# Kernel tuning notes

Hardware: AMD Instinct MI355X
Metric: run time of the kernel (lower is better)

The kernel has to match this reference:

```python
import jax, jax.numpy as jnp
import numpy as np

B, D_in, D_hid, D_out, D_future = 1024, 1024, 1024, 512, 32


def _lin_init(key, out_d, in_d, k_scale):
    k = 1.0 / np.sqrt(k_scale)
    k1, k2 = jax.random.split(key)
    W = jax.random.uniform(k1, (out_d, in_d), minval=-k, maxval=k, dtype=jnp.float32)
    b = jax.random.uniform(k2, (out_d,), minval=-k, maxval=k, dtype=jnp.float32)
    return W, b


def _lstm_cell(x, h, c, W_ih, W_hh, b_ih, b_hh):
    # PyTorch LSTMCell gate order: i, f, g, o
    gates = x @ W_ih.T + b_ih + h @ W_hh.T + b_hh
    i, f, g, o = jnp.split(gates, 4, axis=1)
    c2 = jax.nn.sigmoid(f) * c + jax.nn.sigmoid(i) * jnp.tanh(g)
    h2 = jax.nn.sigmoid(o) * jnp.tanh(c2)
    return h2, c2


def setup_inputs() -> dict:
    key = jax.random.key(0)
    ks = jax.random.split(key, 16)
    x = jax.random.normal(ks[0], (B, D_in), dtype=jnp.float32)
    hx = jax.random.normal(ks[1], (B, D_hid), dtype=jnp.float32)
    cx = jax.random.normal(ks[2], (B, D_hid), dtype=jnp.float32)
    # Decoder LSTMCell(D_out -> D_hid); torch init scale 1/sqrt(hidden)
    W_ih_dec, b_ih_dec = _lin_init(ks[3], 4 * D_hid, D_out, D_hid)
    W_hh_dec, b_hh_dec = _lin_init(ks[4], 4 * D_hid, D_hid, D_hid)
    W_r0, b_r0 = _lin_init(ks[5], D_hid, D_hid, D_hid)
    W_rp, b_rp = _lin_init(ks[6], D_out, D_hid, D_hid)
    W_rr, b_rr = _lin_init(ks[7], D_out, D_out, D_out)
    W_s0, b_s0 = _lin_init(ks[8], D_in, D_hid, D_hid)
    # StaRNNCell LSTMCell(2*D_in -> D_hid)
    W_ih_sta, b_ih_sta = _lin_init(ks[9], 4 * D_hid, 2 * D_in, D_hid)
    W_hh_sta, b_hh_sta = _lin_init(ks[10], 4 * D_hid, D_hid, D_hid)
    W_sn, b_sn = _lin_init(ks[11], D_out, D_hid, D_hid)
    return dict(x=x, hx=hx, cx=cx,
                W_ih_dec=W_ih_dec, W_hh_dec=W_hh_dec, b_ih_dec=b_ih_dec, b_hh_dec=b_hh_dec,
                W_r0=W_r0, b_r0=b_r0, W_rp=W_rp, b_rp=b_rp, W_rr=W_rr, b_rr=b_rr,
                W_s0=W_s0, b_s0=b_s0,
                W_ih_sta=W_ih_sta, W_hh_sta=W_hh_sta, b_ih_sta=b_ih_sta, b_hh_sta=b_hh_sta,
                W_sn=W_sn, b_sn=b_sn)


def reference(x, hx, cx,
              W_ih_dec, W_hh_dec, b_ih_dec, b_hh_dec,
              W_r0, b_r0, W_rp, b_rp, W_rr, b_rr,
              W_s0, b_s0,
              W_ih_sta, W_hh_sta, b_ih_sta, b_hh_sta,
              W_sn, b_sn):
    ohx, ocx = hx, cx
    r0 = jnp.zeros((x.shape[0], D_out), dtype=x.dtype)
    hd0 = hx @ W_r0.T + b_r0  # LinLayerR0

    def step(carry, _):
        r, hd, cd = carry
        hd, cd = _lstm_cell(r, hd, cd, W_ih_dec, W_hh_dec, b_ih_dec, b_hh_dec)
        p = hd @ W_rp.T + b_rp    # LinLayerRp
        r = p @ W_rr.T + b_rr     # LinLayerRr
        return (r, hd, cd), (hd, p)

    _, (fts_bar, Act_bar) = jax.lax.scan(step, (r0, hd0, cx), None, length=D_future)
    # fts_bar: [D_future, B, D_hid]; AvgPool1d over D_future == mean over axis 0
    hbar = fts_bar.mean(axis=0)
    xbar = jax.nn.relu(hbar @ W_s0.T + b_s0)  # LinLayerS0 + relu
    xcat = jnp.concatenate([x, xbar], axis=1)
    hx2, cx2 = _lstm_cell(xcat, ohx, ocx, W_ih_sta, W_hh_sta, b_ih_sta, b_hh_sta)
    Act = hx2 @ W_sn.T + b_sn  # LinLayerSn
    return (Act, Act_bar, (hx2, cx2))
```

## Files before the change

kernel.cpp:

```cpp
#include <hip/hip_runtime.h>
#include <hip/hip_bf16.h>
#include <stdint.h>


typedef unsigned short ushort_t;
typedef __attribute__((ext_vector_type(8))) short short8;
typedef __attribute__((ext_vector_type(4))) float floatx4;

__device__ __forceinline__ unsigned short f2bf(float f) {
    unsigned int u = __float_as_uint(f);
    u += 0x7FFF + ((u >> 16) & 1);
    return (unsigned short)(u >> 16);
}
__device__ __forceinline__ float bf2f(unsigned short u) {
    return __uint_as_float(((unsigned int)u) << 16);
}
__device__ __forceinline__ float sigm(float x) { return 1.f / (1.f + __expf(-x)); }

__device__ __forceinline__ void glds16(const ushort_t* g, const ushort_t* l) {
    __builtin_amdgcn_global_load_lds(
        (const __attribute__((address_space(1))) uint32_t*)g,
        (__attribute__((address_space(3))) uint32_t*)l, 16, 0, 0);
}

template <bool WF, bool WB, bool RELU, bool NT>
__global__ __launch_bounds__(256)
void gemm_bt(const ushort_t* __restrict__ A, int lda,
             const ushort_t* __restrict__ Bw, int ldb,
             int Kloop, int kzOff,
             const float* __restrict__ bias,
             float* __restrict__ Cf, int ldcf, size_t czStride,
             ushort_t* __restrict__ Cb, int ldcb) {
    __shared__ __align__(16) ushort_t As[128 * 32];
    __shared__ __align__(16) ushort_t Bs[128 * 32];
    const int t = threadIdx.x;
    const int l = t & 63;
    const int w = t >> 6;
    int bx = blockIdx.x, by = blockIdx.y;
    if ((gridDim.y & 7) == 0) {
        const int flat = bx + gridDim.x * by;
        const int xcd = flat & 7;
        const int j = flat >> 3;
        const int jm = j / gridDim.x;
        by = xcd * (gridDim.y >> 3) + jm;
        bx = j - jm * gridDim.x;
    }
    const int m0 = by << 7;
    const int n0 = bx << 7;
    const int kz = blockIdx.z;
    A  += (size_t)kz * kzOff;
    Bw += (size_t)kz * kzOff;
    if (WF) Cf += (size_t)kz * czStride;
    const int wm = (w >> 1) << 6;
    const int wn = (w & 1) << 6;
    const int lr = l & 15;
    const int lg = l >> 4;

    floatx4 acc[4][4] = {};

    const int srow = (w << 4) + (l >> 2);
    const int cc = ((l & 3) - ((l >> 3) & 3)) & 3;
    const int scol = cc << 3;
    const ushort_t* Ag0 = A + (size_t)(m0 + srow) * lda + scol;
    const ushort_t* Ag1 = A + (size_t)(m0 + 64 + srow) * lda + scol;
    const ushort_t* Bg0 = Bw + (size_t)(n0 + srow) * ldb + scol;
    const ushort_t* Bg1 = Bw + (size_t)(n0 + 64 + srow) * ldb + scol;
    const ushort_t* lA0 = &As[t * 8];
    const ushort_t* lA1 = &As[2048 + t * 8];
    const ushort_t* lB0 = &Bs[t * 8];
    const ushort_t* lB1 = &Bs[2048 + t * 8];

    int aoff[4], boff[4];
#pragma unroll
    for (int i = 0; i < 4; i++) {
        const int Ra = wm + i * 16 + lr;
        aoff[i] = ((Ra << 2) + ((lg + ((Ra >> 1) & 3)) & 3)) << 3;
        const int Rb = wn + i * 16 + lr;
        boff[i] = ((Rb << 2) + ((lg + ((Rb >> 1) & 3)) & 3)) << 3;
    }

    for (int kk = 0; kk < Kloop; kk += 32) {
        glds16(Ag0 + kk, lA0);
        glds16(Ag1 + kk, lA1);
        glds16(Bg0 + kk, lB0);
        glds16(Bg1 + kk, lB1);
        __syncthreads();
        short8 af[4], bfr[4];
#pragma unroll
        for (int i = 0; i < 4; i++) af[i] = *(const short8*)&As[aoff[i]];
#pragma unroll
        for (int j = 0; j < 4; j++) bfr[j] = *(const short8*)&Bs[boff[j]];
#pragma unroll
        for (int i = 0; i < 4; i++)
#pragma unroll
            for (int j = 0; j < 4; j++)
                acc[i][j] = __builtin_amdgcn_mfma_f32_16x16x32_bf16(af[i], bfr[j], acc[i][j], 0, 0, 0);
        __syncthreads();
    }

#pragma unroll
    for (int i = 0; i < 4; i++) {
#pragma unroll
        for (int j = 0; j < 4; j++) {
            const int col = n0 + wn + j * 16 + lr;
            const float bv = bias ? bias[col] : 0.f;
#pragma unroll
            for (int r = 0; r < 4; r++) {
                const int row = m0 + wm + i * 16 + lg * 4 + r;
                float v = acc[i][j][r] + bv;
                if (RELU) v = fmaxf(v, 0.f);
                if (WF) {
                    if (NT) __builtin_nontemporal_store(v, &Cf[(size_t)row * ldcf + col]);
                    else Cf[(size_t)row * ldcf + col] = v;
                }
                if (WB) Cb[(size_t)row * ldcb + col] = f2bf(v);
            }
        }
    }
}

template <bool HF, bool NT>
__global__ __launch_bounds__(256, 2)
void gates_fused(const ushort_t* __restrict__ A, int lda,
                 const ushort_t* __restrict__ WI, int K,
                 const float* __restrict__ biasI,
                 const float* __restrict__ cin, float* __restrict__ cout,
                 ushort_t* __restrict__ hbf, int ldh,
                 float* __restrict__ hf) {
    __shared__ __align__(16) float Cs[64 * 132];
    ushort_t* AsBase = (ushort_t*)Cs;
    const int t = threadIdx.x;
    const int l = t & 63;
    const int w = t >> 6;
    const int flat = blockIdx.x + (blockIdx.y << 5);
    const int xcd = flat & 7;
    const int jsw = flat >> 3;
    const int bn = (xcd << 2) + (jsw >> 4);
    const int bm = jsw & 15;
    const int m0 = bm << 6;
    const int n0 = bn << 7;
    const int u0 = bn << 5;
    const int lr = l & 15;
    const int lg = l >> 4;

    floatx4 acc[4][2] = {};

    const int srow = t >> 2;
    const int cc = ((t & 3) - ((t >> 3) & 3)) & 3;
    const int scol = cc << 3;
    const ushort_t* Ag = A + (size_t)(m0 + srow) * lda + scol;

    int aoff[4];
#pragma unroll
    for (int i = 0; i < 4; i++) {
        const int Ra = i * 16 + lr;
        aoff[i] = ((Ra << 2) + ((lg + ((Ra >> 1) & 3)) & 3)) << 3;
    }
    const ushort_t* BgW[2];
#pragma unroll
    for (int jf = 0; jf < 2; jf++)
        BgW[jf] = WI + (size_t)(n0 + (w << 5) + jf * 16 + lr) * K + (lg << 3);

    auto issueA = [&](int b, int sp) {
#pragma unroll
        for (int s = 0; s < 4; s++)
            glds16(Ag + sp * 128 + s * 32, AsBase + b * 8192 + s * 2048 + t * 8);
    };
    auto loadB = [&](short8 (&br)[4][2], int sp) {
#pragma unroll
        for (int s = 0; s < 4; s++)
#pragma unroll
            for (int jf = 0; jf < 2; jf++)
                br[s][jf] = *(const short8*)(BgW[jf] + sp * 128 + s * 32);
    };
    auto compute = [&](int b, short8 (&br)[4][2]) {
#pragma unroll
        for (int s = 0; s < 4; s++) {
            short8 af[4];
#pragma unroll
            for (int i = 0; i < 4; i++)
                af[i] = *(const short8*)(AsBase + b * 8192 + s * 2048 + aoff[i]);
#pragma unroll
            for (int i = 0; i < 4; i++)
#pragma unroll
                for (int jf = 0; jf < 2; jf++)
                    acc[i][jf] = __builtin_amdgcn_mfma_f32_16x16x32_bf16(af[i], br[s][jf], acc[i][jf], 0, 0, 0);
        }
    };

    short8 b0[4][2], b1[4][2];
    const int NS = K >> 7;
    issueA(0, 0);
    loadB(b0, 0);
    for (int sp = 0; sp < NS; sp += 2) {
        __syncthreads();
        if (sp + 1 < NS) { issueA(1, sp + 1); loadB(b1, sp + 1); }
        compute(0, b0);
        __syncthreads();
        if (sp + 2 < NS) { issueA(0, sp + 2); loadB(b0, sp + 2); }
        compute(1, b1);
    }
    __syncthreads();

#pragma unroll
    for (int i = 0; i < 4; i++)
#pragma unroll
        for (int jf = 0; jf < 2; jf++) {
            const int colb = (w << 5) + jf * 16 + lr;
#pragma unroll
            for (int r = 0; r < 4; r++)
                Cs[(i * 16 + lg * 4 + r) * 132 + colb] = acc[i][jf][r];
        }
    __syncthreads();

#pragma unroll
    for (int p = 0; p < 8; p++) {
        const int row = p * 8 + (t >> 5);
        const int uu = t & 31;
        const float4 g4 = *(const float4*)&Cs[row * 132 + uu * 4];
        const int grow = m0 + row;
        const int gu = u0 + uu;
        const float4 b4 = *(const float4*)&biasI[gu * 4];
        const float iv = sigm(g4.x + b4.x);
        const float fv = sigm(g4.y + b4.y);
        const float gv = tanhf(g4.z + b4.z);
        const float ov = sigm(g4.w + b4.w);
        const size_t cidx = (size_t)grow * 1024 + gu;
        const float c = fv * cin[cidx] + iv * gv;
        const float h = ov * tanhf(c);
        if (NT) __builtin_nontemporal_store(c, &cout[cidx]);
        else cout[cidx] = c;
        hbf[(size_t)grow * ldh + gu] = f2bf(h);
        if (HF) {
            if (NT) __builtin_nontemporal_store(h, &hf[cidx]);
            else hf[cidx] = h;
        }
    }
}

__global__ void pack2_bf(ushort_t* __restrict__ dst, const float* __restrict__ s1, int K1,
                         const float* __restrict__ s2, int K2) {
    const int n = blockIdx.y;
    const int k = blockIdx.x * 256 + threadIdx.x;
    const int Kt = K1 + K2;
    float v = (k < K1) ? s1[(size_t)n * K1 + k] : s2[(size_t)n * K2 + (k - K1)];
    dst[(size_t)n * Kt + k] = f2bf(v);
}

__global__ void tpose_bf(ushort_t* __restrict__ dst, const float* __restrict__ src,
                         int R, int C) {
    const int c = blockIdx.y;
    const int r = blockIdx.x * 256 + threadIdx.x;
    dst[(size_t)c * R + r] = f2bf(src[(size_t)r * C + c]);
}

__global__ void ileave_whh_k(ushort_t* __restrict__ dst, const float* __restrict__ Whh) {
    const int rI = blockIdx.y;
    const int k = blockIdx.x * 256 + threadIdx.x;
    const int r = ((rI & 3) << 10) + (rI >> 2);
    dst[(size_t)rI * 1024 + k] = f2bf(Whh[(size_t)r * 1024 + k]);
}

__global__ void ileave_add_k(ushort_t* __restrict__ dst, const float* __restrict__ Wgf,
                             const float* __restrict__ Whh) {
    const int rI = blockIdx.y;
    const int k = blockIdx.x * 256 + threadIdx.x;
    const int r = ((rI & 3) << 10) + (rI >> 2);
    dst[(size_t)rI * 1024 + k] = f2bf(Wgf[(size_t)r * 1024 + k] + Whh[(size_t)r * 1024 + k]);
}

__global__ void ileave_sta_k(ushort_t* __restrict__ dst, const float* __restrict__ Wih,
                             const float* __restrict__ Whh) {
    const int rI = blockIdx.y;
    const int k = blockIdx.x * 256 + threadIdx.x;
    const int r = ((rI & 3) << 10) + (rI >> 2);
    float v = (k < 2048) ? Wih[(size_t)r * 2048 + k] : Whh[(size_t)r * 1024 + (k - 2048)];
    dst[(size_t)rI * 3072 + k] = f2bf(v);
}

__global__ void bias_il_k(float* __restrict__ dst, const float* __restrict__ b_ih,
                          const float* __restrict__ b_hh) {
    const int rI = blockIdx.x * 256 + threadIdx.x;
    const int r = ((rI & 3) << 10) + (rI >> 2);
    dst[rI] = b_ih[r] + b_hh[r];
}

__global__ void br2_k(float* __restrict__ br2, const float* __restrict__ Wrr,
                      const float* __restrict__ b_rp, const float* __restrict__ b_rr) {
    const int o = blockIdx.x * 256 + threadIdx.x;
    float s = b_rr[o];
    for (int m = 0; m < 512; m++) s += Wrr[o * 512 + m] * b_rp[m];
    br2[o] = s;
}

__global__ void biasg_k(float* __restrict__ dst, const float* __restrict__ Wih,
                        const float* __restrict__ b_ih, const float* __restrict__ b_hh,
                        const float* __restrict__ br2) {
    const int rI = blockIdx.x * 256 + threadIdx.x;
    const int r = ((rI & 3) << 10) + (rI >> 2);
    float s = b_ih[r] + b_hh[r];
    for (int o = 0; o < 512; o++) s += Wih[(size_t)r * 512 + o] * br2[o];
    dst[rI] = s;
}

__global__ void init_dec(const float* __restrict__ cx, float* __restrict__ cd) {
    int idx = blockIdx.x * 256 + threadIdx.x;
    cd[idx] = cx[idx];
}

__global__ void init_sta(const float* __restrict__ x, const float* __restrict__ hx,
                         ushort_t* __restrict__ A2) {
    int idx = blockIdx.x * 256 + threadIdx.x;
    int b = idx >> 10, j = idx & 1023;
    A2[(size_t)b * 3072 + j] = f2bf(x[idx]);
    A2[(size_t)b * 3072 + 2048 + j] = f2bf(hx[idx]);
}

__global__ void hbar_from_slots(const ushort_t* __restrict__ HD1,
                                ushort_t* __restrict__ out) {
    const size_t SLOT = 1048576;
    int idx = blockIdx.x * 256 + threadIdx.x;
    float s = 0.f;
#pragma unroll 8
    for (int t = 0; t < 32; t++) s += bf2f(HD1[(size_t)t * SLOT + idx]);
    out[idx] = f2bf(s * (1.f / 32.f));
}

extern "C" void kernel_launch(void* const* d_in, const int* in_sizes, int n_in,
                              void* d_out, int out_size, void* d_ws, size_t ws_size,
                              hipStream_t stream) {
    const float* x        = (const float*)d_in[0];
    const float* hx       = (const float*)d_in[1];
    const float* cx       = (const float*)d_in[2];
    const float* W_ih_dec = (const float*)d_in[3];
    const float* W_hh_dec = (const float*)d_in[4];
    const float* b_ih_dec = (const float*)d_in[5];
    const float* b_hh_dec = (const float*)d_in[6];
    const float* W_r0     = (const float*)d_in[7];
    const float* b_r0     = (const float*)d_in[8];
    const float* W_rp     = (const float*)d_in[9];
    const float* b_rp     = (const float*)d_in[10];
    const float* W_rr     = (const float*)d_in[11];
    const float* b_rr     = (const float*)d_in[12];
    const float* W_s0     = (const float*)d_in[13];
    const float* b_s0     = (const float*)d_in[14];
    const float* W_ih_sta = (const float*)d_in[15];
    const float* W_hh_sta = (const float*)d_in[16];
    const float* b_ih_sta = (const float*)d_in[17];
    const float* b_hh_sta = (const float*)d_in[18];
    const float* W_sn     = (const float*)d_in[19];
    const float* b_sn     = (const float*)d_in[20];
    float* out = (float*)d_out;

    float* Act    = out;
    float* ActBar = out + 524288;
    float* Hx2    = out + 524288 + 16777216;
    float* Cx2    = Hx2 + 1048576;

    char* ws = (char*)d_ws;
    size_t off = 0;
    auto alloc = [&](size_t bytes) -> void* {
        void* p = ws + off;
        off += (bytes + 255) & ~(size_t)255;
        return p;
    };
    const size_t SLOT = 1048576;
    ushort_t* HDall  = (ushort_t*)alloc(33ull * SLOT * 2);
    ushort_t* WgI    = (ushort_t*)alloc(4096ull * 1024 * 2);
    ushort_t* WcatSI = (ushort_t*)alloc(4096ull * 3072 * 2);
    ushort_t* Wrpb   = (ushort_t*)alloc(512ull * 1024 * 2);
    ushort_t* Wr0b   = (ushort_t*)alloc(1024ull * 1024 * 2);
    ushort_t* Ws0b   = (ushort_t*)alloc(1024ull * 1024 * 2);
    ushort_t* Wsnb   = (ushort_t*)alloc(512ull * 1024 * 2);
    float*    biasDI = (float*)alloc(4096 * 4);
    float*    biasGI = (float*)alloc(4096 * 4);
    float*    biasSI = (float*)alloc(4096 * 4);
    float*    br2    = (float*)alloc(512 * 4);
    ushort_t* Acat2  = (ushort_t*)alloc(1024ull * 3072 * 2);
    float*    cd     = (float*)alloc(1024ull * 1024 * 4);
    ushort_t* hbarb  = (ushort_t*)alloc(1024ull * 1024 * 2);
    ushort_t* hx2b   = (ushort_t*)alloc(1024ull * 1024 * 2);
    if (ws_size < off) return;

    float*    Wgf    = (float*)(HDall + 1 * SLOT);
    ushort_t* Wihb   = HDall + 9 * SLOT;
    ushort_t* WrpT   = HDall + 11 * SLOT;
    ushort_t* Wrp2Tb = HDall + 11 * SLOT + 524288;
    ushort_t* Wrrb   = HDall + 12 * SLOT;
    ushort_t* WhhI   = HDall + 13 * SLOT;

    init_dec<<<4096, 256, 0, stream>>>(cx, cd);
    init_sta<<<4096, 256, 0, stream>>>(x, hx, Acat2);
    pack2_bf<<<dim3(2, 512), 256, 0, stream>>>(Wrrb, W_rr, 512, nullptr, 0);
    pack2_bf<<<dim3(2, 4096), 256, 0, stream>>>(Wihb, W_ih_dec, 512, nullptr, 0);
    pack2_bf<<<dim3(4, 512), 256, 0, stream>>>(Wrpb, W_rp, 1024, nullptr, 0);
    pack2_bf<<<dim3(4, 1024), 256, 0, stream>>>(Wr0b, W_r0, 1024, nullptr, 0);
    pack2_bf<<<dim3(4, 1024), 256, 0, stream>>>(Ws0b, W_s0, 1024, nullptr, 0);
    pack2_bf<<<dim3(4, 512), 256, 0, stream>>>(Wsnb, W_sn, 1024, nullptr, 0);
    tpose_bf<<<dim3(2, 1024), 256, 0, stream>>>(WrpT, W_rp, 512, 1024);
    ileave_whh_k<<<dim3(4, 4096), 256, 0, stream>>>(WhhI, W_hh_dec);
    bias_il_k<<<16, 256, 0, stream>>>(biasDI, b_ih_dec, b_hh_dec);
    ileave_sta_k<<<dim3(12, 4096), 256, 0, stream>>>(WcatSI, W_ih_sta, W_hh_sta);
    bias_il_k<<<16, 256, 0, stream>>>(biasSI, b_ih_sta, b_hh_sta);
    br2_k<<<2, 256, 0, stream>>>(br2, W_rr, b_rp, b_rr);
    biasg_k<<<16, 256, 0, stream>>>(biasGI, W_ih_dec, b_ih_dec, b_hh_dec, br2);

    gemm_bt<false, true, false, false><<<dim3(4, 8, 1), 256, 0, stream>>>(
        WrpT, 512, Wrrb, 512, 512, 0, nullptr, nullptr, 0, 0, Wrp2Tb, 512);
    gemm_bt<true, false, false, false><<<dim3(8, 32, 1), 256, 0, stream>>>(
        Wihb, 512, Wrp2Tb, 512, 512, 0, nullptr, Wgf, 1024, 0, nullptr, 0);
    ileave_add_k<<<dim3(4, 4096), 256, 0, stream>>>(WgI, Wgf, W_hh_dec);

    gemm_bt<false, true, false, false><<<dim3(8, 8, 1), 256, 0, stream>>>(
        Acat2 + 2048, 3072, Wr0b, 1024, 1024, 0, b_r0, nullptr, 0, 0, HDall, 1024);

    for (int s = 0; s < 32; s++) {
        const ushort_t* WI = (s == 0) ? WhhI : WgI;
        const float* bI = (s == 0) ? biasDI : biasGI;
        gates_fused<false, false><<<dim3(32, 16), 256, 0, stream>>>(
            HDall + (size_t)s * SLOT, 1024, WI, 1024, bI,
            cd, cd, HDall + (size_t)(s + 1) * SLOT, 1024, nullptr);
    }

    gemm_bt<true, false, false, true><<<dim3(4, 256, 1), 256, 0, stream>>>(
        HDall + SLOT, 1024, Wrpb, 1024, 1024, 0, b_rp, ActBar, 512, 0, nullptr, 0);

    hbar_from_slots<<<4096, 256, 0, stream>>>(HDall + SLOT, hbarb);
    gemm_bt<false, true, true, false><<<dim3(8, 8, 1), 256, 0, stream>>>(
        hbarb, 1024, Ws0b, 1024, 1024, 0, b_s0, nullptr, 0, 0, Acat2 + 1024, 3072);

    gates_fused<true, true><<<dim3(32, 16), 256, 0, stream>>>(
        Acat2, 3072, WcatSI, 3072, biasSI, cx, Cx2, hx2b, 1024, Hx2);

    gemm_bt<true, false, false, true><<<dim3(4, 8, 1), 256, 0, stream>>>(
        hx2b, 1024, Wsnb, 1024, 1024, 0, b_sn, Act, 512, 0, nullptr, 0);

    (void)in_sizes; (void)n_in; (void)out_size;
}
```

Baseline: 1.238 ms.

## Replace per-step LSTM gate launches with a persistent kernel using grid barriers

The 32 sequential gate-kernel launches become one persistent kernel of 512 blocks that synchronises between timesteps with a global atomic barrier. The cell state stays in registers across steps, and the hidden-state mean is summed in registers, so the cell-state buffer round-trips, the init copy kernel and the separate hbar reduction kernel go away. This removes launch gaps and memory traffic, but it needs all 512 blocks to be co-resident (launch bounds 256,2) or the barrier deadlocks. Barrier latency is paid on every step.

```diff
diff --git a/kernel.cpp b/kernel.cpp
--- a/kernel.cpp
+++ b/kernel.cpp
@@ -21,6 +21,24 @@
     __builtin_amdgcn_global_load_lds(
         (const __attribute__((address_space(1))) uint32_t*)g,
         (__attribute__((address_space(3))) uint32_t*)l, 16, 0, 0);
+}
+
+__device__ __forceinline__ void grid_sync(unsigned* cnt, unsigned* gen) {
+    __syncthreads();
+    if (threadIdx.x == 0) {
+        __threadfence();
+        unsigned g = __hip_atomic_load(gen, __ATOMIC_RELAXED, __HIP_MEMORY_SCOPE_AGENT);
+        unsigned a = __hip_atomic_fetch_add(cnt, 1u, __ATOMIC_ACQ_REL, __HIP_MEMORY_SCOPE_AGENT);
+        if (a == 511u) {
+            __hip_atomic_store(cnt, 0u, __ATOMIC_RELAXED, __HIP_MEMORY_SCOPE_AGENT);
+            __hip_atomic_store(gen, g + 1u, __ATOMIC_RELEASE, __HIP_MEMORY_SCOPE_AGENT);
+        } else {
+            while (__hip_atomic_load(gen, __ATOMIC_ACQUIRE, __HIP_MEMORY_SCOPE_AGENT) == g)
+                __builtin_amdgcn_s_sleep(8);
+        }
+        __threadfence();
+    }
+    __syncthreads();
 }
 
 template <bool WF, bool WB, bool RELU, bool NT>
@@ -238,6 +256,145 @@
     }
 }
 
+__global__ __launch_bounds__(256, 2)
+void gates_persist(ushort_t* __restrict__ HD,
+                   const ushort_t* __restrict__ Wh,
+                   const ushort_t* __restrict__ Wg,
+                   const float* __restrict__ biasD,
+                   const float* __restrict__ biasG,
+                   const float* __restrict__ cx,
+                   ushort_t* __restrict__ hbarb,
+                   unsigned* __restrict__ bar_cnt, unsigned* __restrict__ bar_gen) {
+    const size_t SLOT = 1048576;
+    __shared__ __align__(16) float Cs[64 * 132];
+    ushort_t* AsBase = (ushort_t*)Cs;
+    const int t = threadIdx.x;
+    const int l = t & 63;
+    const int w = t >> 6;
+    const int flat = blockIdx.x;
+    const int xcd = flat & 7;
+    const int jsw = flat >> 3;
+    const int bn = (xcd << 2) + (jsw >> 4);
+    const int bm = jsw & 15;
+    const int m0 = bm << 6;
+    const int n0 = bn << 7;
+    const int u0 = bn << 5;
+    const int lr = l & 15;
+    const int lg = l >> 4;
+
+    const int srow = t >> 2;
+    const int cc = ((t & 3) - ((t >> 3) & 3)) & 3;
+    const int scol = cc << 3;
+    const ushort_t* Ag = HD + (size_t)(m0 + srow) * 1024 + scol;
+
+    int aoff[4];
+#pragma unroll
+    for (int i = 0; i < 4; i++) {
+        const int Ra = i * 16 + lr;
+        aoff[i] = ((Ra << 2) + ((lg + ((Ra >> 1) & 3)) & 3)) << 3;
+    }
+
+    const int uu = t & 31;
+    const int gu = u0 + uu;
+    const int rb = t >> 5;
+    const float4 b4d = *(const float4*)&biasD[gu * 4];
+    const float4 b4g = *(const float4*)&biasG[gu * 4];
+    float cst[8], hsum[8];
+#pragma unroll
+    for (int p = 0; p < 8; p++) {
+        cst[p] = cx[(size_t)(m0 + p * 8 + rb) * 1024 + gu];
+        hsum[p] = 0.f;
+    }
+
+    for (int s = 0; s < 32; ++s) {
+        if (s) grid_sync(bar_cnt, bar_gen);
+
+        const ushort_t* W = s ? Wg : Wh;
+        const ushort_t* BgW[2];
+#pragma unroll
+        for (int jf = 0; jf < 2; jf++)
+            BgW[jf] = W + (size_t)(n0 + (w << 5) + jf * 16 + lr) * 1024 + (lg << 3);
+
+        floatx4 acc[4][2] = {};
+
+        auto issueA = [&](int b, int sp) {
+#pragma unroll
+            for (int ss = 0; ss < 4; ss++)
+                glds16(Ag + sp * 128 + ss * 32, AsBase + b * 8192 + ss * 2048 + t * 8);
+        };
+        auto loadB = [&](short8 (&br)[4][2], int sp) {
+#pragma unroll
+            for (int ss = 0; ss < 4; ss++)
+#pragma unroll
+                for (int jf = 0; jf < 2; jf++)
+                    br[ss][jf] = *(const short8*)(BgW[jf] + sp * 128 + ss * 32);
+        };
+        auto compute = [&](int b, short8 (&br)[4][2]) {
+#pragma unroll
+            for (int ss = 0; ss < 4; ss++) {
+                short8 af[4];
+#pragma unroll
+                for (int i = 0; i < 4; i++)
+                    af[i] = *(const short8*)(AsBase + b * 8192 + ss * 2048 + aoff[i]);
+#pragma unroll
+                for (int i = 0; i < 4; i++)
+#pragma unroll
+                    for (int jf = 0; jf < 2; jf++)
+                        acc[i][jf] = __builtin_amdgcn_mfma_f32_16x16x32_bf16(af[i], br[ss][jf], acc[i][jf], 0, 0, 0);
+            }
+        };
+
+        short8 b0[4][2], b1[4][2];
+        issueA(0, 0);
+        loadB(b0, 0);
+        for (int sp = 0; sp < 8; sp += 2) {
+            __syncthreads();
+            if (sp + 1 < 8) { issueA(1, sp + 1); loadB(b1, sp + 1); }
+            compute(0, b0);
+            __syncthreads();
+            if (sp + 2 < 8) { issueA(0, sp + 2); loadB(b0, sp + 2); }
+            compute(1, b1);
+        }
+        __syncthreads();
+
+#pragma unroll
+        for (int i = 0; i < 4; i++)
+#pragma unroll
+            for (int jf = 0; jf < 2; jf++) {
+                const int colb = (w << 5) + jf * 16 + lr;
+#pragma unroll
+                for (int r = 0; r < 4; r++)
+                    Cs[(i * 16 + lg * 4 + r) * 132 + colb] = acc[i][jf][r];
+            }
+        __syncthreads();
+
+        ushort_t* Hout = HD + (size_t)(s + 1) * SLOT;
+        const float4 b4 = s ? b4g : b4d;
+#pragma unroll
+        for (int p = 0; p < 8; p++) {
+            const int row = p * 8 + rb;
+            const float4 g4 = *(const float4*)&Cs[row * 132 + uu * 4];
+            const float iv = sigm(g4.x + b4.x);
+            const float fv = sigm(g4.y + b4.y);
+            const float gv = tanhf(g4.z + b4.z);
+            const float ov = sigm(g4.w + b4.w);
+            cst[p] = fv * cst[p] + iv * gv;
+            const float h = ov * tanhf(cst[p]);
+            Hout[(size_t)(m0 + row) * 1024 + gu] = f2bf(h);
+            hsum[p] += h;
+        }
+        Ag += SLOT;
+    }
+
+#pragma unroll
+    for (int p = 0; p < 8; p++)
+        hbarb[(size_t)(m0 + p * 8 + rb) * 1024 + gu] = f2bf(hsum[p] * (1.f / 32.f));
+}
+
+__global__ void zero_bar(unsigned* __restrict__ b) {
+    b[0] = 0u; b[1] = 0u;
+}
+
 __global__ void pack2_bf(ushort_t* __restrict__ dst, const float* __restrict__ s1, int K1,
                          const float* __restrict__ s2, int K2) {
     const int n = blockIdx.y;
@@ -303,27 +460,12 @@
     dst[rI] = s;
 }
 
-__global__ void init_dec(const float* __restrict__ cx, float* __restrict__ cd) {
-    int idx = blockIdx.x * 256 + threadIdx.x;
-    cd[idx] = cx[idx];
-}
-
 __global__ void init_sta(const float* __restrict__ x, const float* __restrict__ hx,
                          ushort_t* __restrict__ A2) {
     int idx = blockIdx.x * 256 + threadIdx.x;
     int b = idx >> 10, j = idx & 1023;
     A2[(size_t)b * 3072 + j] = f2bf(x[idx]);
     A2[(size_t)b * 3072 + 2048 + j] = f2bf(hx[idx]);
-}
-
-__global__ void hbar_from_slots(const ushort_t* __restrict__ HD1,
-                                ushort_t* __restrict__ out) {
-    const size_t SLOT = 1048576;
-    int idx = blockIdx.x * 256 + threadIdx.x;
-    float s = 0.f;
-#pragma unroll 8
-    for (int t = 0; t < 32; t++) s += bf2f(HD1[(size_t)t * SLOT + idx]);
-    out[idx] = f2bf(s * (1.f / 32.f));
 }
 
 extern "C" void kernel_launch(void* const* d_in, const int* in_sizes, int n_in,
@@ -377,9 +519,9 @@
     float*    biasSI = (float*)alloc(4096 * 4);
     float*    br2    = (float*)alloc(512 * 4);
     ushort_t* Acat2  = (ushort_t*)alloc(1024ull * 3072 * 2);
-    float*    cd     = (float*)alloc(1024ull * 1024 * 4);
     ushort_t* hbarb  = (ushort_t*)alloc(1024ull * 1024 * 2);
     ushort_t* hx2b   = (ushort_t*)alloc(1024ull * 1024 * 2);
+    unsigned* barws  = (unsigned*)alloc(256);
     if (ws_size < off) return;
 
     float*    Wgf    = (float*)(HDall + 1 * SLOT);
@@ -389,7 +531,7 @@
     ushort_t* Wrrb   = HDall + 12 * SLOT;
     ushort_t* WhhI   = HDall + 13 * SLOT;
 
-    init_dec<<<4096, 256, 0, stream>>>(cx, cd);
+    zero_bar<<<1, 1, 0, stream>>>(barws);
     init_sta<<<4096, 256, 0, stream>>>(x, hx, Acat2);
     pack2_bf<<<dim3(2, 512), 256, 0, stream>>>(Wrrb, W_rr, 512, nullptr, 0);
     pack2_bf<<<dim3(2, 4096), 256, 0, stream>>>(Wihb, W_ih_dec, 512, nullptr, 0);
@@ -414,18 +556,12 @@
     gemm_bt<false, true, false, false><<<dim3(8, 8, 1), 256, 0, stream>>>(
         Acat2 + 2048, 3072, Wr0b, 1024, 1024, 0, b_r0, nullptr, 0, 0, HDall, 1024);
 
-    for (int s = 0; s < 32; s++) {
-        const ushort_t* WI = (s == 0) ? WhhI : WgI;
-        const float* bI = (s == 0) ? biasDI : biasGI;
-        gates_fused<false, false><<<dim3(32, 16), 256, 0, stream>>>(
-            HDall + (size_t)s * SLOT, 1024, WI, 1024, bI,
-            cd, cd, HDall + (size_t)(s + 1) * SLOT, 1024, nullptr);
-    }
+    gates_persist<<<512, 256, 0, stream>>>(
+        HDall, WhhI, WgI, biasDI, biasGI, cx, hbarb, barws, barws + 1);
 
     gemm_bt<true, false, false, true><<<dim3(4, 256, 1), 256, 0, stream>>>(
         HDall + SLOT, 1024, Wrpb, 1024, 1024, 0, b_rp, ActBar, 512, 0, nullptr, 0);
 
-    hbar_from_slots<<<4096, 256, 0, stream>>>(HDall + SLOT, hbarb);
     gemm_bt<false, true, true, false><<<dim3(8, 8, 1), 256, 0, stream>>>(
         hbarb, 1024, Ws0b, 1024, 1024, 0, b_s0, nullptr, 0, 0, Acat2 + 1024, 3072);
 
```

Measured after the change: 3.065 ms. 2.48x slower.
